# Optimization experiments

Hardware: AMD Instinct MI355X
Metric: run time of the kernel (lower is better)

The kernel has to match this reference:

```python
import jax, jax.numpy as jnp
import numpy as np

SCALE = 16.0
TEMP = 0.07
EPS = 1e-8


def setup_inputs() -> dict:
    key = jax.random.key(0)
    k0, k1, k2, k3, k4 = jax.random.split(key, 5)
    B, D, h, w = 16, 128, 48, 48
    feats_a = jax.random.normal(k0, (B, D, h, w), jnp.float32)
    feats_b = jax.random.normal(k1, (B, D, h, w), jnp.float32)
    eye = jnp.eye(3, dtype=jnp.float32)
    # near-identity homographies (must be invertible)
    Hs_a = eye[None] + 0.02 * jax.random.normal(k2, (B, 3, 3), jnp.float32)
    Hs_b = eye[None] + 0.02 * jax.random.normal(k3, (B, 3, 3), jnp.float32)
    # near-identity affine with a small translation (in large-image pixels)
    M_a_b = jnp.array([[1.0, 0.0, 24.0], [0.0, 1.0, -16.0]], jnp.float32) \
        + 0.01 * jax.random.normal(k4, (2, 3), jnp.float32)
    return {"feats_a": feats_a, "feats_b": feats_b, "Hs_a": Hs_a, "Hs_b": Hs_b, "M_a_b": M_a_b}


def _transform_matrix(Hs_a, Hs_b, M_a_b):
    # Feat_A -> Img_A -> Large_A -> Large_B -> Img_B -> Feat_B
    B = Hs_a.shape[0]
    dt = Hs_a.dtype
    M3 = jnp.concatenate([M_a_b, jnp.array([[0.0, 0.0, 1.0]], dt)], axis=0)  # (3,3)
    S = jnp.diag(jnp.array([SCALE, SCALE, 1.0], dt))
    S_inv = jnp.diag(jnp.array([1.0 / SCALE, 1.0 / SCALE, 1.0], dt))
    Ha_inv = jnp.linalg.inv(Hs_a)  # (B,3,3)
    T = S_inv[None] @ Hs_b @ M3[None] @ Ha_inv @ S[None]
    return T


def _bilinear_sample(feats, grid):
    # feats (B,D,H,W); grid (B,h,w,2) normalized to [-1,1], align_corners=True,
    # zero padding for out-of-range samples (matches F.grid_sample).
    B, D, H, W = feats.shape
    h, w = grid.shape[1], grid.shape[2]
    ix = (grid[..., 0] + 1.0) * 0.5 * (W - 1)  # (B,h,w)
    iy = (grid[..., 1] + 1.0) * 0.5 * (H - 1)
    x0 = jnp.floor(ix); y0 = jnp.floor(iy)
    wx1 = ix - x0; wx0 = 1.0 - wx1
    wy1 = iy - y0; wy0 = 1.0 - wy1
    feats_flat = feats.reshape(B, D, H * W)

    def gather(xi, yi):
        valid = (xi >= 0) & (xi <= W - 1) & (yi >= 0) & (yi <= H - 1)
        xc = jnp.clip(xi, 0, W - 1).astype(jnp.int32)
        yc = jnp.clip(yi, 0, H - 1).astype(jnp.int32)
        idx = (yc * W + xc).reshape(B, -1)  # (B, h*w)
        v = jnp.take_along_axis(feats_flat, idx[:, None, :], axis=2)  # (B,D,h*w)
        return v * valid.reshape(B, 1, -1).astype(feats.dtype)

    out = (gather(x0, y0) * (wx0 * wy0).reshape(B, 1, -1)
           + gather(x0 + 1, y0) * (wx1 * wy0).reshape(B, 1, -1)
           + gather(x0, y0 + 1) * (wx0 * wy1).reshape(B, 1, -1)
           + gather(x0 + 1, y0 + 1) * (wx1 * wy1).reshape(B, 1, -1))
    return out.reshape(B, D, h, w)


def reference(feats_a, feats_b, Hs_a, Hs_b, M_a_b):
    B, D, h, w = feats_a.shape
    N = h * w
    H_b, W_b = feats_b.shape[2], feats_b.shape[3]
    T = _transform_matrix(Hs_a, Hs_b, M_a_b)  # (B,3,3)

    # homogeneous pixel grid of feats_a: (3, N)
    gy, gx = jnp.meshgrid(jnp.arange(h, dtype=jnp.float32), jnp.arange(w, dtype=jnp.float32), indexing='ij')
    coords = jnp.stack([gx.ravel(), gy.ravel(), jnp.ones(N, jnp.float32)], axis=0)  # (3,N)
    new = jnp.einsum('bij,jn->bin', T, coords)  # (B,3,N)
    z = new[:, 2, :] + EPS
    x_norm = 2.0 * (new[:, 0, :] / z) / (W_b - 1) - 1.0  # (B,N)
    y_norm = 2.0 * (new[:, 1, :] / z) / (H_b - 1) - 1.0
    grid = jnp.stack([x_norm, y_norm], axis=-1).reshape(B, h, w, 2)
    valid_mask = ((grid[..., 0] >= -1) & (grid[..., 0] <= 1)
                  & (grid[..., 1] >= -1) & (grid[..., 1] <= 1)).astype(jnp.float32)  # (B,h,w)

    warped_b = _bilinear_sample(feats_b, grid)  # (B,D,h,w)

    fa = feats_a.reshape(B, D, N).transpose(0, 2, 1)   # (B,N,D)
    wb = warped_b.reshape(B, D, N).transpose(0, 2, 1)  # (B,N,D)
    # F.normalize: x / max(||x||, eps) with eps=1e-12
    fa = fa / jnp.maximum(jnp.linalg.norm(fa, axis=2, keepdims=True), 1e-12)
    wb = wb / jnp.maximum(jnp.linalg.norm(wb, axis=2, keepdims=True), 1e-12)

    logits = jnp.einsum('bnd,bmd->bnm', fa, wb) / TEMP  # (B,N,N)
    # cross-entropy with labels = diagonal
    lse = jax.nn.logsumexp(logits, axis=-1)  # (B,N)
    diag = jnp.einsum('bnn->bn', logits)     # (B,N)
    loss_per = lse - diag                    # (B,N)

    mask = valid_mask.reshape(B, N)
    num_valid = mask.sum()
    total = (loss_per * mask).sum()
    return jnp.where(num_valid > 0, total / jnp.maximum(num_valid, 1.0), 0.0)
```

## Files before the change

### kernel.cpp

```cpp
#include <hip/hip_runtime.h>
#include <math.h>

#define B_ 16
#define D_ 128
#define HH 48
#define WW 48
#define N_ 2304
#define SCALE_ 16.0f
#define INV_TEMP 14.285714285714286f
#define EPS_ 1e-8f
#define KP 136

typedef __attribute__((ext_vector_type(8))) short bf16x8;
typedef __attribute__((ext_vector_type(16))) float f32x16;

__device__ __forceinline__ short f2bf(float f) {
    union { float f; unsigned u; } v; v.f = f;
    unsigned r = v.u + 0x7FFFu + ((v.u >> 16) & 1u);
    return (short)(r >> 16);
}

__global__ __launch_bounds__(256) void k_prep(const float* __restrict__ fa,
                                              const float* __restrict__ fb,
                                              const float* __restrict__ Ha,
                                              const float* __restrict__ Hb,
                                              const float* __restrict__ Mab,
                                              float* __restrict__ maskA,
                                              short* __restrict__ faN,
                                              short* __restrict__ wbN) {
    __shared__ float bufA[64][132];
    __shared__ float bufW[64][132];
    __shared__ float part[4][2][64];
    __shared__ float rn[2][64];
    const int b = blockIdx.y;
    const int n0 = blockIdx.x * 64;
    const int tid = threadIdx.x;
    const int nl = tid & 63, dg = tid >> 6;
    const int n = n0 + nl;

    float T[9];
    {
        const float* A = Ha + b * 9;
        const float* Bm = Hb + b * 9;
        float c00 = A[4] * A[8] - A[5] * A[7];
        float c01 = A[5] * A[6] - A[3] * A[8];
        float c02 = A[3] * A[7] - A[4] * A[6];
        float id = 1.f / (A[0] * c00 + A[1] * c01 + A[2] * c02);
        float inv[9] = { c00 * id, (A[2] * A[7] - A[1] * A[8]) * id, (A[1] * A[5] - A[2] * A[4]) * id,
                         c01 * id, (A[0] * A[8] - A[2] * A[6]) * id, (A[2] * A[3] - A[0] * A[5]) * id,
                         c02 * id, (A[1] * A[6] - A[0] * A[7]) * id, (A[0] * A[4] - A[1] * A[3]) * id };
        float M3[9] = {Mab[0], Mab[1], Mab[2], Mab[3], Mab[4], Mab[5], 0.f, 0.f, 1.f};
        float P1[9], P2[9];
        for (int i = 0; i < 3; ++i)
            for (int j = 0; j < 3; ++j) {
                float s = 0.f;
                for (int k = 0; k < 3; ++k) s += Bm[i * 3 + k] * M3[k * 3 + j];
                P1[i * 3 + j] = s;
            }
        for (int i = 0; i < 3; ++i)
            for (int j = 0; j < 3; ++j) {
                float s = 0.f;
                for (int k = 0; k < 3; ++k) s += P1[i * 3 + k] * inv[k * 3 + j];
                P2[i * 3 + j] = s;
            }
        const float sc[3] = {SCALE_, SCALE_, 1.f};
        for (int i = 0; i < 3; ++i)
            for (int j = 0; j < 3; ++j) T[i * 3 + j] = P2[i * 3 + j] * sc[j] / sc[i];
    }

    const float gx = (float)(n % WW), gy = (float)(n / WW);
    const float X = T[0] * gx + T[1] * gy + T[2];
    const float Y = T[3] * gx + T[4] * gy + T[5];
    const float z = T[6] * gx + T[7] * gy + T[8] + EPS_;
    const float xn = 2.f * (X / z) / (float)(WW - 1) - 1.f;
    const float yn = 2.f * (Y / z) / (float)(HH - 1) - 1.f;
    const float msk = (xn >= -1.f && xn <= 1.f && yn >= -1.f && yn <= 1.f) ? 1.f : 0.f;
    const float ix = (xn + 1.f) * 0.5f * (float)(WW - 1);
    const float iy = (yn + 1.f) * 0.5f * (float)(HH - 1);
    const float x0f = floorf(ix), y0f = floorf(iy);
    const float wx1 = ix - x0f, wx0 = 1.f - wx1;
    const float wy1 = iy - y0f, wy0 = 1.f - wy1;
    int offc[4]; float wgt[4];
    {
        float xs[2] = {x0f, x0f + 1.f}, ys[2] = {y0f, y0f + 1.f};
        float wxs[2] = {wx0, wx1}, wys[2] = {wy0, wy1};
        for (int cy = 0; cy < 2; ++cy)
            for (int cx = 0; cx < 2; ++cx) {
                float xi = xs[cx], yi = ys[cy];
                bool v = xi >= 0.f && xi <= (float)(WW - 1) && yi >= 0.f && yi <= (float)(HH - 1);
                int xc = (int)fminf(fmaxf(xi, 0.f), (float)(WW - 1));
                int yc = (int)fminf(fmaxf(yi, 0.f), (float)(HH - 1));
                offc[cy * 2 + cx] = yc * WW + xc;
                wgt[cy * 2 + cx] = v ? wxs[cx] * wys[cy] : 0.f;
            }
    }
    const float* fab = fa + (size_t)b * D_ * N_;
    const float* fbb = fb + (size_t)b * D_ * N_;
    float sA = 0.f, sW = 0.f;
    for (int dd = 0; dd < 32; ++dd) {
        int d = dg * 32 + dd;
        const float* p = fbb + (size_t)d * N_;
        float w = wgt[0] * p[offc[0]] + wgt[1] * p[offc[1]] + wgt[2] * p[offc[2]] + wgt[3] * p[offc[3]];
        float a = fab[(size_t)d * N_ + n];
        bufA[nl][d] = a;
        bufW[nl][d] = w;
        sA += a * a;
        sW += w * w;
    }
    part[dg][0][nl] = sA;
    part[dg][1][nl] = sW;
    __syncthreads();
    if (tid < 64) {
        float ta = part[0][0][tid] + part[1][0][tid] + part[2][0][tid] + part[3][0][tid];
        float tw = part[0][1][tid] + part[1][1][tid] + part[2][1][tid] + part[3][1][tid];
        rn[0][tid] = 1.f / fmaxf(sqrtf(ta), 1e-12f);
        rn[1][tid] = 1.f / fmaxf(sqrtf(tw), 1e-12f);
        maskA[b * N_ + n] = msk;
    }
    __syncthreads();
    const int c = tid & 15;
    const int r0 = tid >> 4;
    for (int pp = 0; pp < 4; ++pp) {
        int r = pp * 16 + r0;
        float sa = rn[0][r], sw = rn[1][r];
        float4 a0 = *(float4*)&bufA[r][c * 8];
        float4 a1 = *(float4*)&bufA[r][c * 8 + 4];
        float4 w0 = *(float4*)&bufW[r][c * 8];
        float4 w1 = *(float4*)&bufW[r][c * 8 + 4];
        bf16x8 oa, ow;
        oa[0] = f2bf(a0.x * sa); oa[1] = f2bf(a0.y * sa); oa[2] = f2bf(a0.z * sa); oa[3] = f2bf(a0.w * sa);
        oa[4] = f2bf(a1.x * sa); oa[5] = f2bf(a1.y * sa); oa[6] = f2bf(a1.z * sa); oa[7] = f2bf(a1.w * sa);
        ow[0] = f2bf(w0.x * sw); ow[1] = f2bf(w0.y * sw); ow[2] = f2bf(w0.z * sw); ow[3] = f2bf(w0.w * sw);
        ow[4] = f2bf(w1.x * sw); ow[5] = f2bf(w1.y * sw); ow[6] = f2bf(w1.z * sw); ow[7] = f2bf(w1.w * sw);
        *(bf16x8*)(faN + (size_t)(b * N_ + n0 + r) * D_ + c * 8) = oa;
        *(bf16x8*)(wbN + (size_t)(b * N_ + n0 + r) * D_ + c * 8) = ow;
    }
}

__global__ __launch_bounds__(256) void k_loss(const float* __restrict__ maskA,
                                              const short* __restrict__ faN,
                                              const short* __restrict__ wbN,
                                              float* __restrict__ acc) {
    __shared__ short a_t[64 * KP];
    __shared__ short b_t[64 * KP];
    __shared__ float s_Z[64];
    __shared__ float s_dg[64];
    const int bx = blockIdx.x, b = blockIdx.y;
    const int tid = threadIdx.x;
    const int n0 = bx * 64;
    const int c = tid & 15, r0 = tid >> 4;

    for (int p = 0; p < 4; ++p) {
        int r = p * 16 + r0;
        bf16x8 v = *(const bf16x8*)(faN + (size_t)(b * N_ + n0 + r) * D_ + c * 8);
        *(bf16x8*)(a_t + r * KP + c * 8) = v;
    }
    if (tid < 64) { s_Z[tid] = 0.f; s_dg[tid] = 0.f; }
    __syncthreads();

    const int lane = tid & 63;
    const int wv = tid >> 6;
    const int rq = wv >> 1, cq = wv & 1;
    const int l31 = lane & 31, h = lane >> 5;

    bf16x8 afr[8];
    {
        const short* ap = a_t + (rq * 32 + l31) * KP + h * 8;
        for (int ks = 0; ks < 8; ++ks) afr[ks] = *(const bf16x8*)(ap + ks * 16);
    }
    float Z[16];
    for (int i = 0; i < 16; ++i) Z[i] = 0.f;

    for (int jt = 0; jt < N_ / 64; ++jt) {
        __syncthreads();
        for (int p = 0; p < 4; ++p) {
            int r = p * 16 + r0;
            bf16x8 v = *(const bf16x8*)(wbN + (size_t)(b * N_ + jt * 64 + r) * D_ + c * 8);
            *(bf16x8*)(b_t + r * KP + c * 8) = v;
        }
        __syncthreads();

        const short* bp = b_t + (cq * 32 + l31) * KP + h * 8;
        f32x16 C;
        for (int i = 0; i < 16; ++i) C[i] = 0.f;
        for (int ks = 0; ks < 8; ++ks) {
            bf16x8 bfr = *(const bf16x8*)(bp + ks * 16);
            C = __builtin_amdgcn_mfma_f32_32x32x16_bf16(afr[ks], bfr, C, 0, 0, 0);
        }
        for (int i = 0; i < 16; ++i)
            Z[i] += __expf(INV_TEMP * C[i] - INV_TEMP);

        if (jt == bx) {
            int gcol_l = cq * 32 + l31;
            for (int i = 0; i < 16; ++i) {
                int rl = rq * 32 + (i & 3) + 8 * (i >> 2) + 4 * h;
                if (gcol_l == rl) s_dg[rl] = INV_TEMP * C[i];
            }
        }
    }
    for (int i = 0; i < 16; ++i) {
        float zz = Z[i];
        zz += __shfl_xor(zz, 1);
        zz += __shfl_xor(zz, 2);
        zz += __shfl_xor(zz, 4);
        zz += __shfl_xor(zz, 8);
        zz += __shfl_xor(zz, 16);
        Z[i] = zz;
    }
    if (l31 == 0) {
        for (int i = 0; i < 16; ++i) {
            int rl = rq * 32 + (i & 3) + 8 * (i >> 2) + 4 * h;
            atomicAdd(&s_Z[rl], Z[i]);
        }
    }
    __syncthreads();
    if (tid < 64) {
        float m = maskA[b * N_ + n0 + tid];
        float lossv = (logf(s_Z[tid]) + INV_TEMP - s_dg[tid]) * m;
        float cm = m;
        for (int off = 1; off < 64; off <<= 1) {
            lossv += __shfl_xor(lossv, off);
            cm += __shfl_xor(cm, off);
        }
        if (tid == 0) {
            atomicAdd(&acc[0], lossv);
            atomicAdd(&acc[1], cm);
        }
    }
}

__global__ void k_final(const float* __restrict__ acc, float* __restrict__ out) {
    float t = acc[0], c = acc[1];
    out[0] = (c > 0.f) ? t / fmaxf(c, 1.f) : 0.f;
}

extern "C" void kernel_launch(void* const* d_in, const int* in_sizes, int n_in,
                              void* d_out, int out_size, void* d_ws, size_t ws_size,
                              hipStream_t stream) {
    const float* fa = (const float*)d_in[0];
    const float* fb = (const float*)d_in[1];
    const float* Ha = (const float*)d_in[2];
    const float* Hb = (const float*)d_in[3];
    const float* M = (const float*)d_in[4];
    float* out = (float*)d_out;

    float* wsf = (float*)d_ws;
    float* accp = wsf;
    float* maskA = wsf + 4;
    short* faN = (short*)(wsf + 4 + B_ * N_);
    short* wbN = faN + (size_t)B_ * N_ * D_;

    hipMemsetAsync(accp, 0, 2 * sizeof(float), stream);
    hipLaunchKernelGGL(k_prep, dim3(N_ / 64, B_), dim3(256), 0, stream,
                       fa, fb, Ha, Hb, M, maskA, faN, wbN);
    hipLaunchKernelGGL(k_loss, dim3(N_ / 64, B_), dim3(256), 0, stream,
                       maskA, faN, wbN, accp);
    hipLaunchKernelGGL(k_final, dim3(1), dim3(1), 0, stream, accp, out);
}
```

Baseline: 150.8 us.

## Split loss column loop across blocks and widen prep to 512 threads

The loss kernel's 36 column tiles are split into 4 chunks handled by separate blocks. Each block atomically adds its partial row sums into a global Z buffer, and a new pass-2 kernel computes the log, mask and reduction. This raises the grid from 576 to 2304 blocks to improve occupancy and latency hiding. The prep kernel now uses 512 threads and stages bf16 values in transposed shared memory, and exp is rewritten as exp2 with an fma. The cost is an extra kernel launch, a larger memset, global float atomics, and double bf16 rounding of features before normalisation.

```diff
diff --git a/kernel.cpp b/kernel.cpp
--- a/kernel.cpp
+++ b/kernel.cpp
@@ -8,8 +8,11 @@
 #define N_ 2304
 #define SCALE_ 16.0f
 #define INV_TEMP 14.285714285714286f
+#define L2E_TEMP 20.60992915555662f
 #define EPS_ 1e-8f
 #define KP 136
+#define SPLIT 4
+#define JT_PER 9
 
 typedef __attribute__((ext_vector_type(8))) short bf16x8;
 typedef __attribute__((ext_vector_type(16))) float f32x16;
@@ -19,8 +22,13 @@
     unsigned r = v.u + 0x7FFFu + ((v.u >> 16) & 1u);
     return (short)(r >> 16);
 }
-
-__global__ __launch_bounds__(256) void k_prep(const float* __restrict__ fa,
+__device__ __forceinline__ float bf2f(short s) {
+    union { unsigned u; float f; } v;
+    v.u = ((unsigned)(unsigned short)s) << 16;
+    return v.f;
+}
+
+__global__ __launch_bounds__(512) void k_prep(const float* __restrict__ fa,
                                               const float* __restrict__ fb,
                                               const float* __restrict__ Ha,
                                               const float* __restrict__ Hb,
@@ -28,9 +36,9 @@
                                               float* __restrict__ maskA,
                                               short* __restrict__ faN,
                                               short* __restrict__ wbN) {
-    __shared__ float bufA[64][132];
-    __shared__ float bufW[64][132];
-    __shared__ float part[4][2][64];
+    __shared__ short sbA[D_][65];
+    __shared__ short sbW[D_][65];
+    __shared__ float part[8][2][64];
     __shared__ float rn[2][64];
     const int b = blockIdx.y;
     const int n0 = blockIdx.x * 64;
@@ -80,30 +88,31 @@
     const float x0f = floorf(ix), y0f = floorf(iy);
     const float wx1 = ix - x0f, wx0 = 1.f - wx1;
     const float wy1 = iy - y0f, wy0 = 1.f - wy1;
-    int offc[4]; float wgt[4];
-    {
-        float xs[2] = {x0f, x0f + 1.f}, ys[2] = {y0f, y0f + 1.f};
-        float wxs[2] = {wx0, wx1}, wys[2] = {wy0, wy1};
-        for (int cy = 0; cy < 2; ++cy)
-            for (int cx = 0; cx < 2; ++cx) {
-                float xi = xs[cx], yi = ys[cy];
-                bool v = xi >= 0.f && xi <= (float)(WW - 1) && yi >= 0.f && yi <= (float)(HH - 1);
-                int xc = (int)fminf(fmaxf(xi, 0.f), (float)(WW - 1));
-                int yc = (int)fminf(fmaxf(yi, 0.f), (float)(HH - 1));
-                offc[cy * 2 + cx] = yc * WW + xc;
-                wgt[cy * 2 + cx] = v ? wxs[cx] * wys[cy] : 0.f;
-            }
-    }
+    const bool vx0 = (x0f >= 0.f) && (x0f <= 47.f);
+    const bool vx1 = (x0f + 1.f >= 0.f) && (x0f + 1.f <= 47.f);
+    const bool vy0 = (y0f >= 0.f) && (y0f <= 47.f);
+    const bool vy1 = (y0f + 1.f >= 0.f) && (y0f + 1.f <= 47.f);
+    const float w00 = (vx0 && vy0) ? wx0 * wy0 : 0.f;
+    const float w01 = (vx1 && vy0) ? wx1 * wy0 : 0.f;
+    const float w10 = (vx0 && vy1) ? wx0 * wy1 : 0.f;
+    const float w11 = (vx1 && vy1) ? wx1 * wy1 : 0.f;
+    const int x0c = (int)fminf(fmaxf(x0f, 0.f), 47.f);
+    const int x1c = (int)fminf(fmaxf(x0f + 1.f, 0.f), 47.f);
+    const int y0c = (int)fminf(fmaxf(y0f, 0.f), 47.f);
+    const int y1c = (int)fminf(fmaxf(y0f + 1.f, 0.f), 47.f);
+    const int o00 = y0c * WW + x0c, o01 = y0c * WW + x1c;
+    const int o10 = y1c * WW + x0c, o11 = y1c * WW + x1c;
+
     const float* fab = fa + (size_t)b * D_ * N_;
     const float* fbb = fb + (size_t)b * D_ * N_;
     float sA = 0.f, sW = 0.f;
-    for (int dd = 0; dd < 32; ++dd) {
-        int d = dg * 32 + dd;
+    for (int dd = 0; dd < 16; ++dd) {
+        int d = dg * 16 + dd;
         const float* p = fbb + (size_t)d * N_;
-        float w = wgt[0] * p[offc[0]] + wgt[1] * p[offc[1]] + wgt[2] * p[offc[2]] + wgt[3] * p[offc[3]];
+        float w = w00 * p[o00] + w01 * p[o01] + w10 * p[o10] + w11 * p[o11];
         float a = fab[(size_t)d * N_ + n];
-        bufA[nl][d] = a;
-        bufW[nl][d] = w;
+        sbA[d][nl] = f2bf(a);
+        sbW[d][nl] = f2bf(w);
         sA += a * a;
         sW += w * w;
     }
@@ -111,55 +120,49 @@
     part[dg][1][nl] = sW;
     __syncthreads();
     if (tid < 64) {
-        float ta = part[0][0][tid] + part[1][0][tid] + part[2][0][tid] + part[3][0][tid];
-        float tw = part[0][1][tid] + part[1][1][tid] + part[2][1][tid] + part[3][1][tid];
+        float ta = 0.f, tw = 0.f;
+        for (int g = 0; g < 8; ++g) { ta += part[g][0][tid]; tw += part[g][1][tid]; }
         rn[0][tid] = 1.f / fmaxf(sqrtf(ta), 1e-12f);
         rn[1][tid] = 1.f / fmaxf(sqrtf(tw), 1e-12f);
-        maskA[b * N_ + n] = msk;
-    }
-    __syncthreads();
-    const int c = tid & 15;
-    const int r0 = tid >> 4;
-    for (int pp = 0; pp < 4; ++pp) {
-        int r = pp * 16 + r0;
+        maskA[b * N_ + n0 + tid] = msk;
+    }
+    __syncthreads();
+    const int c = tid & 15, rr = tid >> 4;
+    for (int p2 = 0; p2 < 2; ++p2) {
+        int r = rr + p2 * 32;
         float sa = rn[0][r], sw = rn[1][r];
-        float4 a0 = *(float4*)&bufA[r][c * 8];
-        float4 a1 = *(float4*)&bufA[r][c * 8 + 4];
-        float4 w0 = *(float4*)&bufW[r][c * 8];
-        float4 w1 = *(float4*)&bufW[r][c * 8 + 4];
         bf16x8 oa, ow;
-        oa[0] = f2bf(a0.x * sa); oa[1] = f2bf(a0.y * sa); oa[2] = f2bf(a0.z * sa); oa[3] = f2bf(a0.w * sa);
-        oa[4] = f2bf(a1.x * sa); oa[5] = f2bf(a1.y * sa); oa[6] = f2bf(a1.z * sa); oa[7] = f2bf(a1.w * sa);
-        ow[0] = f2bf(w0.x * sw); ow[1] = f2bf(w0.y * sw); ow[2] = f2bf(w0.z * sw); ow[3] = f2bf(w0.w * sw);
-        ow[4] = f2bf(w1.x * sw); ow[5] = f2bf(w1.y * sw); ow[6] = f2bf(w1.z * sw); ow[7] = f2bf(w1.w * sw);
+        for (int j = 0; j < 8; ++j) {
+            oa[j] = f2bf(bf2f(sbA[c * 8 + j][r]) * sa);
+            ow[j] = f2bf(bf2f(sbW[c * 8 + j][r]) * sw);
+        }
         *(bf16x8*)(faN + (size_t)(b * N_ + n0 + r) * D_ + c * 8) = oa;
         *(bf16x8*)(wbN + (size_t)(b * N_ + n0 + r) * D_ + c * 8) = ow;
     }
 }
 
-__global__ __launch_bounds__(256) void k_loss(const float* __restrict__ maskA,
-                                              const short* __restrict__ faN,
+__global__ __launch_bounds__(256) void k_loss(const short* __restrict__ faN,
                                               const short* __restrict__ wbN,
-                                              float* __restrict__ acc) {
+                                              float* __restrict__ Zbuf,
+                                              float* __restrict__ dgbuf) {
     __shared__ short a_t[64 * KP];
     __shared__ short b_t[64 * KP];
     __shared__ float s_Z[64];
     __shared__ float s_dg[64];
-    const int bx = blockIdx.x, b = blockIdx.y;
+    const int bx = blockIdx.x, cs = blockIdx.y, b = blockIdx.z;
     const int tid = threadIdx.x;
     const int n0 = bx * 64;
     const int c = tid & 15, r0 = tid >> 4;
 
     for (int p = 0; p < 4; ++p) {
         int r = p * 16 + r0;
-        bf16x8 v = *(const bf16x8*)(faN + (size_t)(b * N_ + n0 + r) * D_ + c * 8);
-        *(bf16x8*)(a_t + r * KP + c * 8) = v;
+        *(bf16x8*)(a_t + r * KP + c * 8) =
+            *(const bf16x8*)(faN + (size_t)(b * N_ + n0 + r) * D_ + c * 8);
     }
     if (tid < 64) { s_Z[tid] = 0.f; s_dg[tid] = 0.f; }
     __syncthreads();
 
-    const int lane = tid & 63;
-    const int wv = tid >> 6;
+    const int lane = tid & 63, wv = tid >> 6;
     const int rq = wv >> 1, cq = wv & 1;
     const int l31 = lane & 31, h = lane >> 5;
 
@@ -170,13 +173,15 @@
     }
     float Z[16];
     for (int i = 0; i < 16; ++i) Z[i] = 0.f;
-
-    for (int jt = 0; jt < N_ / 64; ++jt) {
+    const bool hasDiag = (bx / JT_PER == cs);
+
+    for (int q = 0; q < JT_PER; ++q) {
+        const int jt = cs * JT_PER + q;
         __syncthreads();
         for (int p = 0; p < 4; ++p) {
             int r = p * 16 + r0;
-            bf16x8 v = *(const bf16x8*)(wbN + (size_t)(b * N_ + jt * 64 + r) * D_ + c * 8);
-            *(bf16x8*)(b_t + r * KP + c * 8) = v;
+            *(bf16x8*)(b_t + r * KP + c * 8) =
+                *(const bf16x8*)(wbN + (size_t)(b * N_ + jt * 64 + r) * D_ + c * 8);
         }
         __syncthreads();
 
@@ -188,7 +193,7 @@
             C = __builtin_amdgcn_mfma_f32_32x32x16_bf16(afr[ks], bfr, C, 0, 0, 0);
         }
         for (int i = 0; i < 16; ++i)
-            Z[i] += __expf(INV_TEMP * C[i] - INV_TEMP);
+            Z[i] += exp2f(fmaf(C[i], L2E_TEMP, -L2E_TEMP));
 
         if (jt == bx) {
             int gcol_l = cq * 32 + l31;
@@ -215,17 +220,30 @@
     }
     __syncthreads();
     if (tid < 64) {
-        float m = maskA[b * N_ + n0 + tid];
-        float lossv = (logf(s_Z[tid]) + INV_TEMP - s_dg[tid]) * m;
-        float cm = m;
-        for (int off = 1; off < 64; off <<= 1) {
-            lossv += __shfl_xor(lossv, off);
-            cm += __shfl_xor(cm, off);
-        }
-        if (tid == 0) {
-            atomicAdd(&acc[0], lossv);
-            atomicAdd(&acc[1], cm);
-        }
+        atomicAdd(&Zbuf[b * N_ + n0 + tid], s_Z[tid]);
+        if (hasDiag) dgbuf[b * N_ + n0 + tid] = s_dg[tid];
+    }
+}
+
+__global__ __launch_bounds__(256) void k_pass2(const float* __restrict__ maskA,
+                                               const float* __restrict__ Zbuf,
+                                               const float* __restrict__ dgbuf,
+                                               float* __restrict__ acc) {
+    const int idx = blockIdx.x * 256 + threadIdx.x;
+    const float m = maskA[idx];
+    float lossv = (logf(Zbuf[idx]) + INV_TEMP - dgbuf[idx]) * m;
+    float cm = m;
+    for (int off = 1; off < 64; off <<= 1) {
+        lossv += __shfl_xor(lossv, off);
+        cm += __shfl_xor(cm, off);
+    }
+    __shared__ float s[8];
+    const int wv = threadIdx.x >> 6;
+    if ((threadIdx.x & 63) == 0) { s[wv * 2] = lossv; s[wv * 2 + 1] = cm; }
+    __syncthreads();
+    if (threadIdx.x == 0) {
+        atomicAdd(&acc[0], s[0] + s[2] + s[4] + s[6]);
+        atomicAdd(&acc[1], s[1] + s[3] + s[5] + s[7]);
     }
 }
 
@@ -246,14 +264,18 @@
 
     float* wsf = (float*)d_ws;
     float* accp = wsf;
-    float* maskA = wsf + 4;
-    short* faN = (short*)(wsf + 4 + B_ * N_);
+    float* Zbuf = wsf + 2;
+    float* dgbuf = Zbuf + B_ * N_;
+    float* maskA = dgbuf + B_ * N_;
+    short* faN = (short*)(maskA + B_ * N_);
     short* wbN = faN + (size_t)B_ * N_ * D_;
 
-    hipMemsetAsync(accp, 0, 2 * sizeof(float), stream);
-    hipLaunchKernelGGL(k_prep, dim3(N_ / 64, B_), dim3(256), 0, stream,
+    hipMemsetAsync(wsf, 0, (2 + B_ * N_) * sizeof(float), stream);
+    hipLaunchKernelGGL(k_prep, dim3(N_ / 64, B_), dim3(512), 0, stream,
                        fa, fb, Ha, Hb, M, maskA, faN, wbN);
-    hipLaunchKernelGGL(k_loss, dim3(N_ / 64, B_), dim3(256), 0, stream,
-                       maskA, faN, wbN, accp);
+    hipLaunchKernelGGL(k_loss, dim3(N_ / 64, SPLIT, B_), dim3(256), 0, stream,
+                       faN, wbN, Zbuf, dgbuf);
+    hipLaunchKernelGGL(k_pass2, dim3(B_ * N_ / 256), dim3(256), 0, stream,
+                       maskA, Zbuf, dgbuf, accp);
     hipLaunchKernelGGL(k_final, dim3(1), dim3(1), 0, stream, accp, out);
 }
```

After: 159.5 us. 1.06x slower.
